# Kernel optimization log

Hardware: AMD Instinct MI355X
Metric: run time of the kernel (lower is better)

Reference implementation:

```python
import jax, jax.numpy as jnp
import numpy as np

B, O, A, H, Z = 4096, 512, 64, 2048, 256
CLAMP = 10.0


def _lin(x, w, b):
    # torch nn.Linear layout: w [out, in]
    return x @ w.T + b


def setup_inputs() -> dict:
    key = jax.random.key(0)
    ks = jax.random.split(key, 24)
    n = jax.random.normal
    s = 0.02
    inp = {
        'x_t': n(ks[0], (B, O), jnp.float32),
        'a_prev': n(ks[1], (B, A), jnp.float32),
        'h_prev': n(ks[2], (B, H), jnp.float32),
        'eps': n(ks[3], (B, Z), jnp.float32),
        # prior_net: Linear(H,H) -> ReLU -> Linear(H, 2Z)
        'prior_w1': n(ks[4], (H, H), jnp.float32) * s,
        'prior_b1': jnp.zeros((H,), jnp.float32),
        'prior_w2': n(ks[5], (2 * Z, H), jnp.float32) * s,
        'prior_b2': jnp.zeros((2 * Z,), jnp.float32),
        # enc_net: Linear(O+H,H) -> ReLU -> Linear(H, 2Z)
        'enc_w1': n(ks[6], (H, O + H), jnp.float32) * s,
        'enc_b1': jnp.zeros((H,), jnp.float32),
        'enc_w2': n(ks[7], (2 * Z, H), jnp.float32) * s,
        'enc_b2': jnp.zeros((2 * Z,), jnp.float32),
        # dec_net: Linear(Z+H,H) -> ReLU -> Linear(H, 2O)
        'dec_w1': n(ks[8], (H, Z + H), jnp.float32) * s,
        'dec_b1': jnp.zeros((H,), jnp.float32),
        'dec_w2': n(ks[9], (2 * O, H), jnp.float32) * s,
        'dec_b2': jnp.zeros((2 * O,), jnp.float32),
        # GRUCell: input = O + A + Z, gates ordered (r, z, n)
        'w_ih': n(ks[10], (3 * H, O + A + Z), jnp.float32) * s,
        'w_hh': n(ks[11], (3 * H, H), jnp.float32) * s,
        'b_ih': jnp.zeros((3 * H,), jnp.float32),
        'b_hh': jnp.zeros((3 * H,), jnp.float32),
    }
    return inp


def vrnn_step(x_t, a_prev, h_prev, eps,
              prior_w1, prior_b1, prior_w2, prior_b2,
              enc_w1, enc_b1, enc_w2, enc_b2,
              dec_w1, dec_b1, dec_w2, dec_b2,
              w_ih, w_hh, b_ih, b_hh):
    # prior stats from h_prev
    prior_stats = _lin(jax.nn.relu(_lin(h_prev, prior_w1, prior_b1)), prior_w2, prior_b2)
    mu_p, logvar_p = jnp.split(prior_stats, 2, axis=-1)

    # encoder on [x, h]
    enc_stats = _lin(jax.nn.relu(_lin(jnp.concatenate([x_t, h_prev], -1), enc_w1, enc_b1)), enc_w2, enc_b2)
    mu_q, logvar_q = jnp.split(enc_stats, 2, axis=-1)
    logvar_q = jnp.clip(logvar_q, -CLAMP, CLAMP)
    std_q = jnp.exp(0.5 * logvar_q)
    z_t = mu_q + eps * std_q  # reparameterization

    # decoder on [z, h]
    dec_out = _lin(jax.nn.relu(_lin(jnp.concatenate([z_t, h_prev], -1), dec_w1, dec_b1)), dec_w2, dec_b2)
    mu_x, logvar_x = jnp.split(dec_out, 2, axis=-1)
    logvar_x = jnp.clip(logvar_x, -CLAMP, CLAMP)
    nll = 0.5 * jnp.sum((x_t - mu_x) ** 2 * jnp.exp(-logvar_x) + logvar_x, axis=-1)

    # KL(q || p), diagonal Gaussians
    var_p = jnp.exp(logvar_p)
    kl = 0.5 * jnp.sum((mu_q - mu_p) ** 2 / var_p + jnp.exp(logvar_q) / var_p
                       + (logvar_p - logvar_q) - 1.0, axis=-1)

    # GRUCell (torch gate order: r, z, n)
    rnn_in = jnp.concatenate([x_t, z_t, a_prev], -1)
    gi = rnn_in @ w_ih.T + b_ih
    gh = h_prev @ w_hh.T + b_hh
    i_r, i_z, i_n = jnp.split(gi, 3, axis=-1)
    h_r, h_z, h_n = jnp.split(gh, 3, axis=-1)
    r = jax.nn.sigmoid(i_r + h_r)
    zg = jax.nn.sigmoid(i_z + h_z)
    n = jnp.tanh(i_n + r * h_n)
    h_t = (1.0 - zg) * n + zg * h_prev

    return h_t, nll, kl, z_t, mu_q, logvar_q


def reference(x_t, a_prev, h_prev, eps,
              prior_w1, prior_b1, prior_w2, prior_b2,
              enc_w1, enc_b1, enc_w2, enc_b2,
              dec_w1, dec_b1, dec_w2, dec_b2,
              w_ih, w_hh, b_ih, b_hh):
    return vrnn_step(x_t, a_prev, h_prev, eps,
                     prior_w1, prior_b1, prior_w2, prior_b2,
                     enc_w1, enc_b1, enc_w2, enc_b2,
                     dec_w1, dec_b1, dec_w2, dec_b2,
                     w_ih, w_hh, b_ih, b_hh)
```

## Files before the change

### kernel.cpp

```cpp
#include <hip/hip_runtime.h>
#include <stdint.h>


#define B_SZ 4096
#define H_SZ 2048
#define Z_SZ 256

typedef __attribute__((ext_vector_type(4))) float f32x4;
typedef __attribute__((ext_vector_type(8))) short s16x8;

__device__ __forceinline__ uint16_t f2b(float f) {
  union { float f; uint32_t u; } v; v.f = f;
  uint32_t u = v.u;
  uint32_t r = (u + 0x7FFFu + ((u >> 16) & 1u)) >> 16;
  return (uint16_t)r;
}
__device__ __forceinline__ float b2f(uint16_t h) {
  union { uint32_t u; float f; } v; v.u = ((uint32_t)h) << 16; return v.f;
}
__device__ __forceinline__ float clip10(float v) { return fminf(fmaxf(v, -10.0f), 10.0f); }

__global__ void convert_kernel(const float* __restrict__ src, uint16_t* __restrict__ dst,
                               int C8, int C, int dstLd, int ngroups) {
  int i = blockIdx.x * 256 + threadIdx.x;
  if (i >= ngroups) return;
  int row = i / C8;
  int cg = i - row * C8;
  const f32x4* s = (const f32x4*)(src + (size_t)row * C + (size_t)cg * 8);
  f32x4 lo = s[0], hi = s[1];
  s16x8 p;
  p[0] = (short)f2b(lo[0]); p[1] = (short)f2b(lo[1]);
  p[2] = (short)f2b(lo[2]); p[3] = (short)f2b(lo[3]);
  p[4] = (short)f2b(hi[0]); p[5] = (short)f2b(hi[1]);
  p[6] = (short)f2b(hi[2]); p[7] = (short)f2b(hi[3]);
  *(s16x8*)(dst + (size_t)row * dstLd + (size_t)cg * 8) = p;
}

__device__ __forceinline__ void gload_lds16(const uint16_t* g, uint16_t* l) {
  __builtin_amdgcn_global_load_lds(
      (const __attribute__((address_space(1))) uint32_t*)g,
      (__attribute__((address_space(3))) uint32_t*)(uintptr_t)(void*)l,
      16, 0, 0);
}

template <int EPI>
__global__ __launch_bounds__(256)
void gemm_bt(const uint16_t* __restrict__ A0, int lda0, int ks1,
             const uint16_t* __restrict__ A1, int lda1, int ks2,
             const uint16_t* __restrict__ A2, int lda2,
             const uint16_t* __restrict__ W,
             const float* __restrict__ bias0, const float* __restrict__ bias1,
             uint16_t* __restrict__ C0, int ldc0, int splitN,
             uint16_t* __restrict__ C1, int ldc1,
             int Nt, int K) {
  __shared__ uint16_t As[128 * 64];
  __shared__ uint16_t Ws[128 * 64];
  int mtile = blockIdx.x / Nt;
  int ntile = blockIdx.x - mtile * Nt;
  const int row0 = mtile << 7, col0 = ntile << 7;
  const int t = threadIdx.x;
  const int w = t >> 6, l = t & 63;
  const int wr = w >> 1, wc = w & 1;
  const int sr = l >> 3, scg = l & 7;
  const int fr = l & 15, fq = l >> 4;

  f32x4 acc[4][4] = {};

  const uint16_t* Wbase = W + (size_t)(col0 + w * 32 + sr) * K + scg * 8;

  for (int k0 = 0; k0 < K; k0 += 64) {
    const uint16_t* ab; int ald, koff;
    if (k0 < ks1)      { ab = A0; ald = lda0; koff = k0; }
    else if (k0 < ks2) { ab = A1; ald = lda1; koff = k0 - ks1; }
    else               { ab = A2; ald = lda2; koff = k0 - ks2; }
    const uint16_t* Abase = ab + (size_t)(row0 + w * 32 + sr) * ald + koff + scg * 8;
#pragma unroll
    for (int j = 0; j < 4; ++j)
      gload_lds16(Abase + (size_t)(j * 8) * ald, &As[(w * 32 + j * 8) * 64]);
#pragma unroll
    for (int j = 0; j < 4; ++j)
      gload_lds16(Wbase + (size_t)(j * 8) * K + k0, &Ws[(w * 32 + j * 8) * 64]);
    __syncthreads();
#pragma unroll
    for (int ks = 0; ks < 2; ++ks) {
      s16x8 fa[4], fb[4];
#pragma unroll
      for (int m = 0; m < 4; ++m)
        fa[m] = *(const s16x8*)&As[(wr * 64 + m * 16 + fr) * 64 + ks * 32 + fq * 8];
#pragma unroll
      for (int n = 0; n < 4; ++n)
        fb[n] = *(const s16x8*)&Ws[(wc * 64 + n * 16 + fr) * 64 + ks * 32 + fq * 8];
#pragma unroll
      for (int m = 0; m < 4; ++m)
#pragma unroll
        for (int n = 0; n < 4; ++n)
          acc[m][n] = __builtin_amdgcn_mfma_f32_16x16x32_bf16(fa[m], fb[n], acc[m][n], 0, 0, 0);
    }
    __syncthreads();
  }

#pragma unroll
  for (int m = 0; m < 4; ++m) {
    int grow = row0 + wr * 64 + m * 16 + fq * 4;
#pragma unroll
    for (int n = 0; n < 4; ++n) {
      int gcol = col0 + wc * 64 + n * 16 + fr;
      bool first = (EPI != 3) || (gcol < splitN);
      float bs = first ? bias0[gcol] : bias1[gcol - splitN];
#pragma unroll
      for (int i = 0; i < 4; ++i) {
        float v = acc[m][n][i] + bs;
        if (EPI == 1 || (EPI == 3 && first)) v = fmaxf(v, 0.0f);
        if (first)
          C0[(size_t)(grow + i) * ldc0 + gcol] = f2b(v);
        else
          C1[(size_t)(grow + i) * ldc1 + (gcol - splitN)] = f2b(v);
      }
    }
  }
}

__global__ void z_kernel_t1(const uint16_t* __restrict__ es, const float* __restrict__ eps,
                            float* __restrict__ oz, float* __restrict__ omu,
                            float* __restrict__ olq, uint16_t* __restrict__ zbuf) {
  int i = blockIdx.x * 256 + threadIdx.x;
  int b = i >> 8, j = i & 255;
  float mu = b2f(es[(size_t)b * 512 + j]);
  float lq = clip10(b2f(es[(size_t)b * 512 + 256 + j]));
  float z = mu + eps[i] * __expf(0.5f * lq);
  oz[i] = z; omu[i] = mu; olq[i] = lq;
  zbuf[i] = f2b(z);
}

__device__ __forceinline__ float block_sum256(float v) {
  __shared__ float ps[4];
#pragma unroll
  for (int o = 32; o > 0; o >>= 1) v += __shfl_xor(v, o, 64);
  int l = threadIdx.x & 63, w = threadIdx.x >> 6;
  if (l == 0) ps[w] = v;
  __syncthreads();
  float r = ps[0] + ps[1] + ps[2] + ps[3];
  __syncthreads();
  return r;
}

__global__ __launch_bounds__(256)
void gru_fused_t1(const uint16_t* __restrict__ gi, const uint16_t* __restrict__ gh,
                  const float* __restrict__ hp, const float* __restrict__ x,
                  const uint16_t* __restrict__ dec, const uint16_t* __restrict__ pst,
                  const uint16_t* __restrict__ es,
                  float* __restrict__ out_h, float* __restrict__ out_nll,
                  float* __restrict__ out_kl) {
  int b = blockIdx.x, t = threadIdx.x;
  size_t gbase = (size_t)b * 6144 + (size_t)t * 8;
  s16x8 ir = *(const s16x8*)(gi + gbase);
  s16x8 iz = *(const s16x8*)(gi + gbase + 2048);
  s16x8 inn = *(const s16x8*)(gi + gbase + 4096);
  s16x8 hr = *(const s16x8*)(gh + gbase);
  s16x8 hz = *(const s16x8*)(gh + gbase + 2048);
  s16x8 hn = *(const s16x8*)(gh + gbase + 4096);
  size_t hbase = (size_t)b * 2048 + (size_t)t * 8;
  f32x4 h0 = *(const f32x4*)(hp + hbase);
  f32x4 h1v = *(const f32x4*)(hp + hbase + 4);
  f32x4 o0, o1;
#pragma unroll
  for (int e = 0; e < 8; ++e) {
    float r = 1.f / (1.f + __expf(-(b2f((uint16_t)ir[e]) + b2f((uint16_t)hr[e]))));
    float zg = 1.f / (1.f + __expf(-(b2f((uint16_t)iz[e]) + b2f((uint16_t)hz[e]))));
    float nv = b2f((uint16_t)inn[e]) + r * b2f((uint16_t)hn[e]);
    float t2 = __expf(-2.f * fabsf(nv));
    float n = (1.f - t2) / (1.f + t2);
    n = (nv >= 0.f) ? n : -n;
    float hv = (e < 4) ? h0[e] : h1v[e - 4];
    float o = (1.f - zg) * n + zg * hv;
    if (e < 4) o0[e] = o; else o1[e - 4] = o;
  }
  *(f32x4*)(out_h + hbase) = o0;
  *(f32x4*)(out_h + hbase + 4) = o1;

  float s = 0.f;
#pragma unroll
  for (int rr = 0; rr < 2; ++rr) {
    int j = t + rr * 256;
    float mu = b2f(dec[(size_t)b * 1024 + j]);
    float lx = clip10(b2f(dec[(size_t)b * 1024 + 512 + j]));
    float d = x[(size_t)b * 512 + j] - mu;
    s += d * d * __expf(-lx) + lx;
  }
  s = block_sum256(s);
  if (t == 0) out_nll[b] = 0.5f * s;

  float mu_p = b2f(pst[(size_t)b * 512 + t]);
  float lp = b2f(pst[(size_t)b * 512 + 256 + t]);
  float mu_q = b2f(es[(size_t)b * 512 + t]);
  float lq = clip10(b2f(es[(size_t)b * 512 + 256 + t]));
  float dq = mu_q - mu_p;
  float enl = __expf(-lp);
  float kv = dq * dq * enl + __expf(lq) * enl + (lp - lq) - 1.0f;
  kv = block_sum256(kv);
  if (t == 0) out_kl[b] = 0.5f * kv;
}

template <int MODE>
__global__ __launch_bounds__(256)
void gemm_nv(const float* __restrict__ A0, int ld0, int s1,
             const float* __restrict__ A1, int ld1, int s2,
             const float* __restrict__ A2, int ld2,
             const float* __restrict__ W, const float* __restrict__ bias,
             float* __restrict__ C, int N, int K) {
  int nb = N >> 8;
  int m = blockIdx.x / nb;
  int n = (blockIdx.x - m * nb) * 256 + threadIdx.x;
  const float* w = W + (size_t)n * K;
  float acc = 0.f;
  int k = 0;
  for (; k < s1; ++k) acc += A0[(size_t)m * ld0 + k] * w[k];
  for (; k < s2; ++k) acc += A1[(size_t)m * ld1 + (k - s1)] * w[k];
  for (; k < K; ++k) acc += A2[(size_t)m * ld2 + (k - s2)] * w[k];
  acc += bias[n];
  if (MODE == 1) acc = fmaxf(acc, 0.f);
  C[(size_t)m * N + n] = acc;
}

__global__ void z_nv(const float* __restrict__ ests, const float* __restrict__ eps,
                     float* __restrict__ oz, float* __restrict__ omu,
                     float* __restrict__ olq, float* __restrict__ zs, int row0, int nR) {
  int i = blockIdx.x * 256 + threadIdx.x;
  if (i >= nR * 256) return;
  int bl = i >> 8, j = i & 255;
  size_t g = (size_t)(row0 + bl) * 256 + j;
  float mu = ests[(size_t)bl * 512 + j];
  float lq = clip10(ests[(size_t)bl * 512 + 256 + j]);
  float z = mu + eps[g] * __expf(0.5f * lq);
  oz[g] = z; omu[g] = mu; olq[g] = lq;
  zs[(size_t)bl * 256 + j] = z;
}

__global__ void nll_nv(const float* __restrict__ x, const float* __restrict__ decs,
                       float* __restrict__ out, int row0) {
  int bl = blockIdx.x, l = threadIdx.x;
  int gb = row0 + bl;
  float s = 0.f;
  for (int j = l; j < 512; j += 64) {
    float mu = decs[(size_t)bl * 1024 + j];
    float lx = clip10(decs[(size_t)bl * 1024 + 512 + j]);
    float d = x[(size_t)gb * 512 + j] - mu;
    s += d * d * __expf(-lx) + lx;
  }
#pragma unroll
  for (int o = 32; o > 0; o >>= 1) s += __shfl_xor(s, o, 64);
  if (l == 0) out[gb] = 0.5f * s;
}

__global__ void kl_nv(const float* __restrict__ psts, const float* __restrict__ ests,
                      float* __restrict__ out, int row0) {
  int bl = blockIdx.x, l = threadIdx.x;
  int gb = row0 + bl;
  float s = 0.f;
  for (int j = l; j < 256; j += 64) {
    float mu_p = psts[(size_t)bl * 512 + j];
    float lp = psts[(size_t)bl * 512 + 256 + j];
    float mu_q = ests[(size_t)bl * 512 + j];
    float lq = clip10(ests[(size_t)bl * 512 + 256 + j]);
    float d = mu_q - mu_p;
    float enl = __expf(-lp);
    s += d * d * enl + __expf(lq) * enl + (lp - lq) - 1.0f;
  }
#pragma unroll
  for (int o = 32; o > 0; o >>= 1) s += __shfl_xor(s, o, 64);
  if (l == 0) out[gb] = 0.5f * s;
}

__global__ void gru_nv(const float* __restrict__ gis, const float* __restrict__ ghs,
                       const float* __restrict__ hp, float* __restrict__ ho,
                       int row0, int nR) {
  int i = blockIdx.x * 256 + threadIdx.x;
  if (i >= nR * 2048) return;
  int bl = i >> 11, j = i & 2047;
  size_t lb = (size_t)bl * 6144 + j;
  float r = 1.f / (1.f + __expf(-(gis[lb] + ghs[lb])));
  float zg = 1.f / (1.f + __expf(-(gis[lb + 2048] + ghs[lb + 2048])));
  float nv = gis[lb + 4096] + r * ghs[lb + 4096];
  float t2 = __expf(-2.f * fabsf(nv));
  float n = (1.f - t2) / (1.f + t2);
  n = (nv >= 0.f) ? n : -n;
  size_t g = (size_t)(row0 + bl) * 2048 + j;
  ho[g] = (1.f - zg) * n + zg * hp[g];
}

extern "C" void kernel_launch(void* const* d_in, const int* in_sizes, int n_in,
                              void* d_out, int out_size, void* d_ws, size_t ws_size,
                              hipStream_t stream) {
  const float* x_t = (const float*)d_in[0];
  const float* a_prev = (const float*)d_in[1];
  const float* h_prev = (const float*)d_in[2];
  const float* eps = (const float*)d_in[3];
  const float* prior_w1 = (const float*)d_in[4];
  const float* prior_b1 = (const float*)d_in[5];
  const float* prior_w2 = (const float*)d_in[6];
  const float* prior_b2 = (const float*)d_in[7];
  const float* enc_w1 = (const float*)d_in[8];
  const float* enc_b1 = (const float*)d_in[9];
  const float* enc_w2 = (const float*)d_in[10];
  const float* enc_b2 = (const float*)d_in[11];
  const float* dec_w1 = (const float*)d_in[12];
  const float* dec_b1 = (const float*)d_in[13];
  const float* dec_w2 = (const float*)d_in[14];
  const float* dec_b2 = (const float*)d_in[15];
  const float* w_ih = (const float*)d_in[16];
  const float* w_hh = (const float*)d_in[17];
  const float* b_ih = (const float*)d_in[18];
  const float* b_hh = (const float*)d_in[19];

  float* out = (float*)d_out;
  float* out_h = out;
  float* out_nll = out + (size_t)B_SZ * H_SZ;
  float* out_kl = out_nll + B_SZ;
  float* out_z = out_kl + B_SZ;
  float* out_mu = out_z + (size_t)B_SZ * Z_SZ;
  float* out_lq = out_mu + (size_t)B_SZ * Z_SZ;

  char* ws = (char*)d_ws;
  size_t off = 0;
  auto alloc = [&](size_t bytes) {
    void* p = ws + off;
    off += (bytes + 255) & ~(size_t)255;
    return p;
  };

  const size_t T1_DEMAND = 179568640;
  if (ws_size >= T1_DEMAND) {
    uint16_t* wcat = (uint16_t*)alloc((size_t)8192 * 2048 * 2);
    uint16_t* pw2 = (uint16_t*)alloc((size_t)512 * 2048 * 2);
    uint16_t* ew1 = (uint16_t*)alloc((size_t)2048 * 2560 * 2);
    uint16_t* ew2 = (uint16_t*)alloc((size_t)512 * 2048 * 2);
    uint16_t* dw1 = (uint16_t*)alloc((size_t)2048 * 2304 * 2);
    uint16_t* dw2 = (uint16_t*)alloc((size_t)1024 * 2048 * 2);
    uint16_t* wih = (uint16_t*)alloc((size_t)6144 * 832 * 2);
    uint16_t* xh = (uint16_t*)alloc((size_t)B_SZ * 2560 * 2);
    uint16_t* zbuf = (uint16_t*)alloc((size_t)B_SZ * 256 * 2);
    uint16_t* abuf = (uint16_t*)alloc((size_t)B_SZ * 64 * 2);
    uint16_t* h1 = (uint16_t*)alloc((size_t)B_SZ * 2048 * 2);
    uint16_t* pstats = (uint16_t*)alloc((size_t)B_SZ * 512 * 2);
    uint16_t* estats = (uint16_t*)alloc((size_t)B_SZ * 512 * 2);
    uint16_t* decout = (uint16_t*)alloc((size_t)B_SZ * 1024 * 2);
    uint16_t* gh = (uint16_t*)alloc((size_t)B_SZ * 6144 * 2);
    uint16_t* gi = wcat;

    auto conv = [&](const float* src, uint16_t* dst, int R, int C, int ld) {
      int ng = R * (C / 8);
      convert_kernel<<<dim3((ng + 255) / 256), dim3(256), 0, stream>>>(src, dst, C / 8, C, ld, ng);
    };
    conv(prior_w1, wcat, 2048, 2048, 2048);
    conv(w_hh, wcat + (size_t)2048 * 2048, 6144, 2048, 2048);
    conv(prior_w2, pw2, 512, 2048, 2048);
    conv(enc_w1, ew1, 2048, 2560, 2560);
    conv(enc_w2, ew2, 512, 2048, 2048);
    conv(dec_w1, dw1, 2048, 2304, 2304);
    conv(dec_w2, dw2, 1024, 2048, 2048);
    conv(w_ih, wih, 6144, 832, 832);
    conv(x_t, xh, B_SZ, 512, 2560);
    conv(h_prev, xh + 512, B_SZ, 2048, 2560);
    conv(a_prev, abuf, B_SZ, 64, 64);

    auto gemm1 = [&](const uint16_t* A, int lda, const uint16_t* W, const float* bias,
                     uint16_t* C, int ldc, int N, int K, int relu) {
      int Nt = N / 128;
      dim3 grid((B_SZ / 128) * Nt);
      if (relu)
        gemm_bt<1><<<grid, dim3(256), 0, stream>>>(A, lda, K, A, lda, K, A, lda, W,
                                                   bias, bias, C, ldc, N, C, ldc, Nt, K);
      else
        gemm_bt<2><<<grid, dim3(256), 0, stream>>>(A, lda, K, A, lda, K, A, lda, W,
                                                   bias, bias, C, ldc, N, C, ldc, Nt, K);
    };

    gemm_bt<3><<<dim3((B_SZ / 128) * 64), dim3(256), 0, stream>>>(
        xh + 512, 2560, 2048, xh, 2560, 2048, xh, 2560, wcat,
        prior_b1, b_hh, h1, 2048, 2048, gh, 6144, 64, 2048);
    gemm1(h1, 2048, pw2, prior_b2, pstats, 512, 512, 2048, 0);
    gemm1(xh, 2560, ew1, enc_b1, h1, 2048, 2048, 2560, 1);
    gemm1(h1, 2048, ew2, enc_b2, estats, 512, 512, 2048, 0);
    z_kernel_t1<<<dim3(B_SZ * Z_SZ / 256), dim3(256), 0, stream>>>(
        estats, eps, out_z, out_mu, out_lq, zbuf);
    gemm_bt<1><<<dim3((B_SZ / 128) * 16), dim3(256), 0, stream>>>(
        zbuf, 256, 256, xh + 512, 2560, 2304, xh, 2560, dw1,
        dec_b1, dec_b1, h1, 2048, 2048, h1, 2048, 16, 2304);
    gemm1(h1, 2048, dw2, dec_b2, decout, 1024, 1024, 2048, 0);
    gemm_bt<2><<<dim3((B_SZ / 128) * 48), dim3(256), 0, stream>>>(
        xh, 2560, 512, zbuf, 256, 768, abuf, 64, wih,
        b_ih, b_ih, gi, 6144, 6144, gi, 6144, 48, 832);
    gru_fused_t1<<<dim3(B_SZ), dim3(256), 0, stream>>>(
        gi, gh, h_prev, x_t, decout, pstats, estats, out_h, out_nll, out_kl);
  } else {
    int R = 512;
    while (R > 32 && (size_t)R * 66560 + 4096 > ws_size) R >>= 1;
    float* h1s = (float*)alloc((size_t)R * 2048 * 4);
    float* psts = (float*)alloc((size_t)R * 512 * 4);
    float* ests = (float*)alloc((size_t)R * 512 * 4);
    float* decs = (float*)alloc((size_t)R * 1024 * 4);
    float* zs = (float*)alloc((size_t)R * 256 * 4);
    float* gis = (float*)alloc((size_t)R * 6144 * 4);
    float* ghs = (float*)alloc((size_t)R * 6144 * 4);
    const float* dummy = x_t;

    auto nv = [&](const float* A0, int ld0, int s1, const float* A1, int ld1, int s2,
                  const float* A2, int ld2, const float* W, const float* bias,
                  float* C, int M, int N, int K, int relu) {
      dim3 grid(M * (N / 256));
      if (relu)
        gemm_nv<1><<<grid, dim3(256), 0, stream>>>(A0, ld0, s1, A1, ld1, s2, A2, ld2, W, bias, C, N, K);
      else
        gemm_nv<0><<<grid, dim3(256), 0, stream>>>(A0, ld0, s1, A1, ld1, s2, A2, ld2, W, bias, C, N, K);
    };

    for (int s = 0; s < B_SZ / R; ++s) {
      int r0 = s * R;
      const float* xs = x_t + (size_t)r0 * 512;
      const float* hs = h_prev + (size_t)r0 * 2048;
      const float* as = a_prev + (size_t)r0 * 64;
      nv(hs, 2048, 2048, dummy, 0, 2048, dummy, 0, prior_w1, prior_b1, h1s, R, 2048, 2048, 1);
      nv(h1s, 2048, 2048, dummy, 0, 2048, dummy, 0, prior_w2, prior_b2, psts, R, 512, 2048, 0);
      nv(xs, 512, 512, hs, 2048, 2560, dummy, 0, enc_w1, enc_b1, h1s, R, 2048, 2560, 1);
      nv(h1s, 2048, 2048, dummy, 0, 2048, dummy, 0, enc_w2, enc_b2, ests, R, 512, 2048, 0);
      z_nv<<<dim3((R * 256 + 255) / 256), dim3(256), 0, stream>>>(
          ests, eps, out_z, out_mu, out_lq, zs, r0, R);
      nv(zs, 256, 256, hs, 2048, 2304, dummy, 0, dec_w1, dec_b1, h1s, R, 2048, 2304, 1);
      nv(h1s, 2048, 2048, dummy, 0, 2048, dummy, 0, dec_w2, dec_b2, decs, R, 1024, 2048, 0);
      nv(hs, 2048, 2048, dummy, 0, 2048, dummy, 0, w_hh, b_hh, ghs, R, 6144, 2048, 0);
      nv(xs, 512, 512, zs, 256, 768, as, 64, w_ih, b_ih, gis, R, 6144, 832, 0);
      nll_nv<<<dim3(R), dim3(64), 0, stream>>>(x_t, decs, out_nll, r0);
      kl_nv<<<dim3(R), dim3(64), 0, stream>>>(psts, ests, out_kl, r0);
      gru_nv<<<dim3((R * 2048 + 255) / 256), dim3(256), 0, stream>>>(
          gis, ghs, h_prev, out_h, r0, R);
    }
  }
}
```

Before: 567.9 us.

## Merge all h_prev-multiplied weight blocks into one wide GEMM and add tile swizzle

Splits the encoder and decoder first-layer weights into their h_prev part and their x or z part. All h_prev-driven products (prior W1, GRU W_hh, encoder W1h, decoder W1h) are concatenated into one 12288-wide GEMM, which leaves small K=512 and K=256 GEMMs that accumulate into the stored pre-activation and then apply ReLU. This removes the repeated reading of h_prev across separate GEMMs and increases the parallelism of the large launch. It also adds a blockIdx swizzle in the GEMM for cache locality. The cost is a bigger workspace requirement and a bf16 round-trip of the partial sums, which may lose some precision.

```diff
diff --git a/kernel.cpp b/kernel.cpp
--- a/kernel.cpp
+++ b/kernel.cpp
@@ -21,12 +21,12 @@
 __device__ __forceinline__ float clip10(float v) { return fminf(fmaxf(v, -10.0f), 10.0f); }
 
 __global__ void convert_kernel(const float* __restrict__ src, uint16_t* __restrict__ dst,
-                               int C8, int C, int dstLd, int ngroups) {
+                               int C8, int srcLd, int dstLd, int ngroups) {
   int i = blockIdx.x * 256 + threadIdx.x;
   if (i >= ngroups) return;
   int row = i / C8;
   int cg = i - row * C8;
-  const f32x4* s = (const f32x4*)(src + (size_t)row * C + (size_t)cg * 8);
+  const f32x4* s = (const f32x4*)(src + (size_t)row * srcLd + (size_t)cg * 8);
   f32x4 lo = s[0], hi = s[1];
   s16x8 p;
   p[0] = (short)f2b(lo[0]); p[1] = (short)f2b(lo[1]);
@@ -34,6 +34,18 @@
   p[4] = (short)f2b(hi[0]); p[5] = (short)f2b(hi[1]);
   p[6] = (short)f2b(hi[2]); p[7] = (short)f2b(hi[3]);
   *(s16x8*)(dst + (size_t)row * dstLd + (size_t)cg * 8) = p;
+}
+
+__global__ void biascat_kernel(const float* __restrict__ b0, const float* __restrict__ b1,
+                               const float* __restrict__ b2, const float* __restrict__ b3,
+                               float* __restrict__ dst) {
+  int j = blockIdx.x * 256 + threadIdx.x;
+  float v;
+  if (j < 2048) v = b0[j];
+  else if (j < 8192) v = b1[j - 2048];
+  else if (j < 10240) v = b2[j - 8192];
+  else v = b3[j - 10240];
+  dst[j] = v;
 }
 
 __device__ __forceinline__ void gload_lds16(const uint16_t* g, uint16_t* l) {
@@ -55,8 +67,10 @@
              int Nt, int K) {
   __shared__ uint16_t As[128 * 64];
   __shared__ uint16_t Ws[128 * 64];
-  int mtile = blockIdx.x / Nt;
-  int ntile = blockIdx.x - mtile * Nt;
+  int nwg = gridDim.x;
+  int swz = (blockIdx.x & 7) * (nwg >> 3) + (blockIdx.x >> 3);
+  int mtile = swz / Nt;
+  int ntile = swz - mtile * Nt;
   const int row0 = mtile << 7, col0 = ntile << 7;
   const int t = threadIdx.x;
   const int w = t >> 6, l = t & 63;
@@ -105,16 +119,32 @@
 #pragma unroll
     for (int n = 0; n < 4; ++n) {
       int gcol = col0 + wc * 64 + n * 16 + fr;
-      bool first = (EPI != 3) || (gcol < splitN);
-      float bs = first ? bias0[gcol] : bias1[gcol - splitN];
 #pragma unroll
       for (int i = 0; i < 4; ++i) {
-        float v = acc[m][n][i] + bs;
-        if (EPI == 1 || (EPI == 3 && first)) v = fmaxf(v, 0.0f);
-        if (first)
-          C0[(size_t)(grow + i) * ldc0 + gcol] = f2b(v);
-        else
-          C1[(size_t)(grow + i) * ldc1 + (gcol - splitN)] = f2b(v);
+        size_t idx0 = (size_t)(grow + i) * ldc0 + gcol;
+        float v = acc[m][n][i];
+        if (EPI == 1) {
+          v = fmaxf(v + bias0[gcol], 0.0f);
+          C0[idx0] = f2b(v);
+        } else if (EPI == 2) {
+          C0[idx0] = f2b(v + bias0[gcol]);
+        } else if (EPI == 3) {
+          bool first = gcol < splitN;
+          float bs = first ? bias0[gcol] : bias1[gcol - splitN];
+          v += bs;
+          if (first) {
+            C0[idx0] = f2b(fmaxf(v, 0.0f));
+          } else {
+            C1[(size_t)(grow + i) * ldc1 + (gcol - splitN)] = f2b(v);
+          }
+        } else if (EPI == 5) {
+          v += bias0[gcol];
+          if (gcol < splitN) v = fmaxf(v, 0.0f);
+          C0[idx0] = f2b(v);
+        } else {
+          v += b2f(C0[idx0]);
+          C0[idx0] = f2b(fmaxf(v, 0.0f));
+        }
       }
     }
   }
@@ -145,20 +175,22 @@
 }
 
 __global__ __launch_bounds__(256)
-void gru_fused_t1(const uint16_t* __restrict__ gi, const uint16_t* __restrict__ gh,
+void gru_fused_t1(const uint16_t* __restrict__ gi, int ldgi,
+                  const uint16_t* __restrict__ gh, int ldgh,
                   const float* __restrict__ hp, const float* __restrict__ x,
                   const uint16_t* __restrict__ dec, const uint16_t* __restrict__ pst,
                   const uint16_t* __restrict__ es,
                   float* __restrict__ out_h, float* __restrict__ out_nll,
                   float* __restrict__ out_kl) {
   int b = blockIdx.x, t = threadIdx.x;
-  size_t gbase = (size_t)b * 6144 + (size_t)t * 8;
-  s16x8 ir = *(const s16x8*)(gi + gbase);
-  s16x8 iz = *(const s16x8*)(gi + gbase + 2048);
-  s16x8 inn = *(const s16x8*)(gi + gbase + 4096);
-  s16x8 hr = *(const s16x8*)(gh + gbase);
-  s16x8 hz = *(const s16x8*)(gh + gbase + 2048);
-  s16x8 hn = *(const s16x8*)(gh + gbase + 4096);
+  size_t gbi = (size_t)b * ldgi + (size_t)t * 8;
+  size_t gbh = (size_t)b * ldgh + (size_t)t * 8;
+  s16x8 ir = *(const s16x8*)(gi + gbi);
+  s16x8 iz = *(const s16x8*)(gi + gbi + 2048);
+  s16x8 inn = *(const s16x8*)(gi + gbi + 4096);
+  s16x8 hr = *(const s16x8*)(gh + gbh);
+  s16x8 hz = *(const s16x8*)(gh + gbh + 2048);
+  s16x8 hn = *(const s16x8*)(gh + gbh + 4096);
   size_t hbase = (size_t)b * 2048 + (size_t)t * 8;
   f32x4 h0 = *(const f32x4*)(hp + hbase);
   f32x4 h1v = *(const f32x4*)(hp + hbase + 4);
@@ -328,8 +360,75 @@
     return p;
   };
 
-  const size_t T1_DEMAND = 179568640;
+  auto conv = [&](const float* src, uint16_t* dst, int R, int C, int srcLd, int dstLd) {
+    int ng = R * (C / 8);
+    convert_kernel<<<dim3((ng + 255) / 256), dim3(256), 0, stream>>>(src, dst, C / 8, srcLd, dstLd, ng);
+  };
+
+  const size_t T1_DEMAND = 194248704 + 65536;
+  const size_t T1B_DEMAND = 179568640;
+
   if (ws_size >= T1_DEMAND) {
+    uint16_t* wmega = (uint16_t*)alloc((size_t)12288 * 2048 * 2);
+    uint16_t* wih = (uint16_t*)alloc((size_t)6144 * 832 * 2);
+    uint16_t* wx_enc = (uint16_t*)alloc((size_t)2048 * 512 * 2);
+    uint16_t* wz_dec = (uint16_t*)alloc((size_t)2048 * 256 * 2);
+    uint16_t* pw2 = (uint16_t*)alloc((size_t)512 * 2048 * 2);
+    uint16_t* ew2 = (uint16_t*)alloc((size_t)512 * 2048 * 2);
+    uint16_t* dw2 = (uint16_t*)alloc((size_t)1024 * 2048 * 2);
+    uint16_t* xbuf = (uint16_t*)alloc((size_t)B_SZ * 512 * 2);
+    uint16_t* hbuf = (uint16_t*)alloc((size_t)B_SZ * 2048 * 2);
+    uint16_t* abuf = (uint16_t*)alloc((size_t)B_SZ * 64 * 2);
+    uint16_t* megaC = (uint16_t*)alloc((size_t)B_SZ * 12288 * 2);
+    float* biascat = (float*)alloc(12288 * 4);
+    uint16_t* gi = wmega;
+    uint16_t* decout = wih;
+    uint16_t* pstats = hbuf;
+    uint16_t* estats = hbuf + (size_t)2097152;
+    uint16_t* zbuf = hbuf + (size_t)4194304;
+
+    conv(prior_w1, wmega, 2048, 2048, 2048, 2048);
+    conv(w_hh, wmega + (size_t)2048 * 2048, 6144, 2048, 2048, 2048);
+    conv(enc_w1 + 512, wmega + (size_t)8192 * 2048, 2048, 2048, 2560, 2048);
+    conv(dec_w1 + 256, wmega + (size_t)10240 * 2048, 2048, 2048, 2304, 2048);
+    conv(enc_w1, wx_enc, 2048, 512, 2560, 512);
+    conv(dec_w1, wz_dec, 2048, 256, 2304, 256);
+    conv(prior_w2, pw2, 512, 2048, 2048, 2048);
+    conv(enc_w2, ew2, 512, 2048, 2048, 2048);
+    conv(dec_w2, dw2, 1024, 2048, 2048, 2048);
+    conv(w_ih, wih, 6144, 832, 832, 832);
+    conv(x_t, xbuf, B_SZ, 512, 512, 512);
+    conv(h_prev, hbuf, B_SZ, 2048, 2048, 2048);
+    conv(a_prev, abuf, B_SZ, 64, 64, 64);
+    biascat_kernel<<<dim3(48), dim3(256), 0, stream>>>(prior_b1, b_hh, enc_b1, dec_b1, biascat);
+
+    gemm_bt<5><<<dim3((B_SZ / 128) * 96), dim3(256), 0, stream>>>(
+        hbuf, 2048, 2048, hbuf, 2048, 2048, hbuf, 2048, wmega,
+        biascat, biascat, megaC, 12288, 2048, megaC, 12288, 96, 2048);
+    gemm_bt<2><<<dim3((B_SZ / 128) * 4), dim3(256), 0, stream>>>(
+        megaC, 12288, 2048, megaC, 12288, 2048, megaC, 12288, pw2,
+        prior_b2, prior_b2, pstats, 512, 512, pstats, 512, 4, 2048);
+    gemm_bt<6><<<dim3((B_SZ / 128) * 16), dim3(256), 0, stream>>>(
+        xbuf, 512, 512, xbuf, 512, 512, xbuf, 512, wx_enc,
+        enc_b1, enc_b1, megaC + 8192, 12288, 2048, megaC + 8192, 12288, 16, 512);
+    gemm_bt<2><<<dim3((B_SZ / 128) * 4), dim3(256), 0, stream>>>(
+        megaC + 8192, 12288, 2048, megaC + 8192, 12288, 2048, megaC + 8192, 12288, ew2,
+        enc_b2, enc_b2, estats, 512, 512, estats, 512, 4, 2048);
+    z_kernel_t1<<<dim3(B_SZ * Z_SZ / 256), dim3(256), 0, stream>>>(
+        estats, eps, out_z, out_mu, out_lq, zbuf);
+    gemm_bt<2><<<dim3((B_SZ / 128) * 48), dim3(256), 0, stream>>>(
+        xbuf, 512, 512, zbuf, 256, 768, abuf, 64, wih,
+        b_ih, b_ih, gi, 6144, 6144, gi, 6144, 48, 832);
+    gemm_bt<6><<<dim3((B_SZ / 128) * 16), dim3(256), 0, stream>>>(
+        zbuf, 256, 256, zbuf, 256, 256, zbuf, 256, wz_dec,
+        dec_b1, dec_b1, megaC + 10240, 12288, 2048, megaC + 10240, 12288, 16, 256);
+    gemm_bt<2><<<dim3((B_SZ / 128) * 8), dim3(256), 0, stream>>>(
+        megaC + 10240, 12288, 2048, megaC + 10240, 12288, 2048, megaC + 10240, 12288, dw2,
+        dec_b2, dec_b2, decout, 1024, 1024, decout, 1024, 8, 2048);
+    gru_fused_t1<<<dim3(B_SZ), dim3(256), 0, stream>>>(
+        gi, 6144, megaC + 2048, 12288, h_prev, x_t, decout, pstats, estats,
+        out_h, out_nll, out_kl);
+  } else if (ws_size >= T1B_DEMAND) {
     uint16_t* wcat = (uint16_t*)alloc((size_t)8192 * 2048 * 2);
     uint16_t* pw2 = (uint16_t*)alloc((size_t)512 * 2048 * 2);
     uint16_t* ew1 = (uint16_t*)alloc((size_t)2048 * 2560 * 2);
@@ -347,21 +446,17 @@
     uint16_t* gh = (uint16_t*)alloc((size_t)B_SZ * 6144 * 2);
     uint16_t* gi = wcat;
 
-    auto conv = [&](const float* src, uint16_t* dst, int R, int C, int ld) {
-      int ng = R * (C / 8);
-      convert_kernel<<<dim3((ng + 255) / 256), dim3(256), 0, stream>>>(src, dst, C / 8, C, ld, ng);
-    };
-    conv(prior_w1, wcat, 2048, 2048, 2048);
-    conv(w_hh, wcat + (size_t)2048 * 2048, 6144, 2048, 2048);
-    conv(prior_w2, pw2, 512, 2048, 2048);
-    conv(enc_w1, ew1, 2048, 2560, 2560);
-    conv(enc_w2, ew2, 512, 2048, 2048);
-    conv(dec_w1, dw1, 2048, 2304, 2304);
-    conv(dec_w2, dw2, 1024, 2048, 2048);
-    conv(w_ih, wih, 6144, 832, 832);
-    conv(x_t, xh, B_SZ, 512, 2560);
-    conv(h_prev, xh + 512, B_SZ, 2048, 2560);
-    conv(a_prev, abuf, B_SZ, 64, 64);
+    conv(prior_w1, wcat, 2048, 2048, 2048, 2048);
+    conv(w_hh, wcat + (size_t)2048 * 2048, 6144, 2048, 2048, 2048);
+    conv(prior_w2, pw2, 512, 2048, 2048, 2048);
+    conv(enc_w1, ew1, 2048, 2560, 2560, 2560);
+    conv(enc_w2, ew2, 512, 2048, 2048, 2048);
+    conv(dec_w1, dw1, 2048, 2304, 2304, 2304);
+    conv(dec_w2, dw2, 1024, 2048, 2048, 2048);
+    conv(w_ih, wih, 6144, 832, 832, 832);
+    conv(x_t, xh, B_SZ, 512, 512, 2560);
+    conv(h_prev, xh + 512, B_SZ, 2048, 2048, 2560);
+    conv(a_prev, abuf, B_SZ, 64, 64, 64);
 
     auto gemm1 = [&](const uint16_t* A, int lda, const uint16_t* W, const float* bias,
                      uint16_t* C, int ldc, int N, int K, int relu) {
@@ -391,7 +486,8 @@
         xh, 2560, 512, zbuf, 256, 768, abuf, 64, wih,
         b_ih, b_ih, gi, 6144, 6144, gi, 6144, 48, 832);
     gru_fused_t1<<<dim3(B_SZ), dim3(256), 0, stream>>>(
-        gi, gh, h_prev, x_t, decout, pstats, estats, out_h, out_nll, out_kl);
+        gi, 6144, gh, 6144, h_prev, x_t, decout, pstats, estats,
+        out_h, out_nll, out_kl);
   } else {
     int R = 512;
     while (R > 32 && (size_t)R * 66560 + 4096 > ws_size) R >>= 1;
```

Result: slower. 594.7 us (+4.7%).
